# Performance work log

Hardware: AMD Instinct MI355X
Metric: run time of the kernel (lower is better)

Reference implementation:

```python
import jax, jax.numpy as jnp
import numpy as np

B, L, D = 16, 8192, 256

def setup_inputs() -> dict:
    key = jax.random.key(0)
    inputs = jax.random.normal(key, (B, L, D), dtype=jnp.float32)
    return {"inputs": inputs}

def reference(inputs) -> jnp.ndarray:
    # position weights: softmax over L of per-token L2 norms
    norms = jnp.linalg.norm(inputs, axis=2)            # [B, L]
    w = jax.nn.softmax(norms, axis=1)                  # [B, L]
    # weighted sum of outer products == X^T diag(w) X, fused as one einsum
    out = jnp.einsum('bl,bld,ble->bde', w, inputs, inputs)  # [B, D, D]
    return out
```

## Files before the change

kernel.cpp:

```cpp
#include <hip/hip_runtime.h>
#include <hip/hip_bf16.h>

#define NB 16
#define NL 8192
#define ND 256
#define KSPLIT 16
#define CHUNK (NL / KSPLIT)
#define BK 64

#define WS_G_OFF 256

typedef __bf16 bf16_t;
typedef __attribute__((ext_vector_type(8))) __bf16 bf16x8;
typedef __attribute__((ext_vector_type(4))) float floatx4;

__device__ __forceinline__ int fsw(int col) {
    return ((col >> 2) & 7) ^ ((col & 3) << 1);
}

__global__ __launch_bounds__(512, 2) void k_gemm(const float* __restrict__ x,
                                                 float* __restrict__ ws,
                                                 float* __restrict__ gram) {
    const int ks = blockIdx.x, b = blockIdx.y;
    const int t = threadIdx.x;
    const int lane = t & 63;
    const int w = __builtin_amdgcn_readfirstlane(t >> 6);
    const int quad = lane >> 4, m = lane & 15;

    __shared__ bf16_t lds[256 * 64];

    const float* xb = x + (size_t)b * NL * ND;
    const int l0 = ks * CHUNK;

    floatx4 accA[9], accB[8];
    #pragma unroll
    for (int j = 0; j < 9; ++j)
        #pragma unroll
        for (int r = 0; r < 4; ++r) accA[j][r] = 0.f;
    #pragma unroll
    for (int j = 0; j < 8; ++j)
        #pragma unroll
        for (int r = 0; r < 4; ++r) accB[j][r] = 0.f;

    float e_acc = 0.f;
    float4 xv[8];

    {
        const float* gp = xb + (size_t)(l0 + w * 8) * ND + lane * 4;
        #pragma unroll
        for (int j = 0; j < 8; ++j) xv[j] = *(const float4*)(gp + (size_t)j * ND);
    }

    for (int kk = 0; kk < CHUNK; kk += BK) {
        if (kk) __syncthreads();
        {
            float ss[8];
            #pragma unroll
            for (int j = 0; j < 8; ++j)
                ss[j] = xv[j].x * xv[j].x + xv[j].y * xv[j].y
                      + xv[j].z * xv[j].z + xv[j].w * xv[j].w;
            #pragma unroll
            for (int off = 32; off; off >>= 1) {
                #pragma unroll
                for (int j = 0; j < 8; ++j) ss[j] += __shfl_xor(ss[j], off, 64);
            }
            float s[8];
            #pragma unroll
            for (int j = 0; j < 8; ++j) {
                s[j] = __expf(0.5f * sqrtf(ss[j]));
                e_acc += s[j] * s[j];
            }
            bf16x8 p[4];
            #pragma unroll
            for (int j = 0; j < 8; ++j) {
                const float* vf = (const float*)&xv[j];
                #pragma unroll
                for (int c = 0; c < 4; ++c) p[c][j] = (bf16_t)(vf[c] * s[j]);
            }
            #pragma unroll
            for (int c = 0; c < 4; ++c) {
                const int col = 4 * lane + c;
                const int chunk = w ^ fsw(col);
                *(bf16x8*)(&lds[col * 64 + chunk * 8]) = p[c];
            }
        }
        __syncthreads();
        if (kk + BK < CHUNK) {
            const float* gp = xb + (size_t)(l0 + kk + BK + w * 8) * ND + lane * 4;
            #pragma unroll
            for (int j = 0; j < 8; ++j) xv[j] = *(const float4*)(gp + (size_t)j * ND);
        }
        #pragma unroll
        for (int k2 = 0; k2 < 2; ++k2) {
            const int kcq = k2 * 4 + quad;
            bf16x8 fB[16];
            #pragma unroll
            for (int j = 0; j < 16; ++j) {
                const int col = (((w + j) & 15) << 4) + m;
                fB[j] = *(const bf16x8*)(&lds[(col << 6) + ((kcq ^ fsw(col)) << 3)]);
            }
            #pragma unroll
            for (int j = 0; j < 9; ++j)
                accA[j] = __builtin_amdgcn_mfma_f32_16x16x32_bf16(fB[0], fB[j], accA[j], 0, 0, 0);
            #pragma unroll
            for (int j = 0; j < 8; ++j)
                accB[j] = __builtin_amdgcn_mfma_f32_16x16x32_bf16(fB[8], fB[8 + j], accB[j], 0, 0, 0);
        }
    }

    __shared__ float red[8];
    if (lane == 0) red[w] = e_acc;
    __syncthreads();
    if (t == 0) {
        float z = 0.f;
        #pragma unroll
        for (int i = 0; i < 8; ++i) z += red[i];
        atomicAdd(&ws[b * 16], z);
    }

    float* gb = gram + (size_t)(ks * NB + b) * 144 * 256;
    #pragma unroll
    for (int j = 0; j < 9; ++j) {
        float* tb = gb + (w * 9 + j) * 256 + quad * 64 + m;
        #pragma unroll
        for (int reg = 0; reg < 4; ++reg) tb[reg * 16] = accA[j][reg];
    }
    #pragma unroll
    for (int j = 0; j < 8; ++j) {
        float* tb = gb + ((w + 8) * 9 + j) * 256 + quad * 64 + m;
        #pragma unroll
        for (int reg = 0; reg < 4; ++reg) tb[reg * 16] = accB[j][reg];
    }
}

__global__ __launch_bounds__(256) void k_reduce(const float* __restrict__ gram,
                                                const float* __restrict__ ws,
                                                float* __restrict__ out) {
    const int gid = blockIdx.x * 256 + threadIdx.x;
    const int elem = gid & 255;
    const int rem  = gid >> 8;
    const int slot = rem % 144;
    const int b    = rem / 144;
    const int rt = slot / 9;
    const int j  = slot - rt * 9;
    if (rt >= 8 && j == 8) return;
    const int ct = (rt + j) & 15;
    float sum = 0.f;
    #pragma unroll
    for (int ks = 0; ks < KSPLIT; ++ks)
        sum += gram[((size_t)(ks * NB + b) * 144 + slot) * 256 + elem];
    sum *= 1.0f / ws[b * 16];
    const int er = elem >> 4, ec = elem & 15;
    const int d = rt * 16 + er, e = ct * 16 + ec;
    float* ob = out + (size_t)b * ND * ND;
    ob[(size_t)d * ND + e] = sum;
    if (j) ob[(size_t)e * ND + d] = sum;
}

extern "C" void kernel_launch(void* const* d_in, const int* in_sizes, int n_in,
                              void* d_out, int out_size, void* d_ws, size_t ws_size,
                              hipStream_t stream) {
    const float* x = (const float*)d_in[0];
    float* out = (float*)d_out;
    float* ws = (float*)d_ws;
    float* gram = ws + WS_G_OFF;

    hipMemsetAsync(d_ws, 0, 1024, stream);
    k_gemm<<<dim3(KSPLIT, NB), 512, 0, stream>>>(x, ws, gram);
    k_reduce<<<dim3(NB * 144 * 256 / 256), 256, 0, stream>>>(gram, ws, out);
}
```

Baseline: 207.7 us.

## Double block to 1024 threads with one row-tile per wave

The GEMM kernel now launches 1024 threads (16 waves) instead of 512. Each wave owns a single 16-row tile with 9 accumulators, where before it owned two tiles with 17. Each wave loads 4 rows instead of 8 and writes bf16x4 halves into the swizzled LDS tile, and B fragments are loaded and consumed one at a time instead of being held as 16 registers. The aim is lower register pressure and more waves to hide latency. In exchange, upper-half waves now compute a redundant ninth (diagonal-opposite) tile, and the reduce kernel is adjusted to write it without transposing.

```diff
diff --git a/kernel.cpp b/kernel.cpp
--- a/kernel.cpp
+++ b/kernel.cpp
@@ -11,6 +11,7 @@
 #define WS_G_OFF 256
 
 typedef __bf16 bf16_t;
+typedef __attribute__((ext_vector_type(4))) __bf16 bf16x4;
 typedef __attribute__((ext_vector_type(8))) __bf16 bf16x8;
 typedef __attribute__((ext_vector_type(4))) float floatx4;
 
@@ -18,61 +19,57 @@
     return ((col >> 2) & 7) ^ ((col & 3) << 1);
 }
 
-__global__ __launch_bounds__(512, 2) void k_gemm(const float* __restrict__ x,
-                                                 float* __restrict__ ws,
-                                                 float* __restrict__ gram) {
+__global__ __launch_bounds__(1024, 4) void k_gemm(const float* __restrict__ x,
+                                                  float* __restrict__ ws,
+                                                  float* __restrict__ gram) {
     const int ks = blockIdx.x, b = blockIdx.y;
     const int t = threadIdx.x;
     const int lane = t & 63;
     const int w = __builtin_amdgcn_readfirstlane(t >> 6);
     const int quad = lane >> 4, m = lane & 15;
+    const int g = w >> 1, h = w & 1;
 
     __shared__ bf16_t lds[256 * 64];
 
     const float* xb = x + (size_t)b * NL * ND;
     const int l0 = ks * CHUNK;
 
-    floatx4 accA[9], accB[8];
+    floatx4 acc[9];
     #pragma unroll
     for (int j = 0; j < 9; ++j)
         #pragma unroll
-        for (int r = 0; r < 4; ++r) accA[j][r] = 0.f;
-    #pragma unroll
-    for (int j = 0; j < 8; ++j)
-        #pragma unroll
-        for (int r = 0; r < 4; ++r) accB[j][r] = 0.f;
+        for (int r = 0; r < 4; ++r) acc[j][r] = 0.f;
 
     float e_acc = 0.f;
-    float4 xv[8];
-
+    float4 xv[4];
     {
-        const float* gp = xb + (size_t)(l0 + w * 8) * ND + lane * 4;
+        const float* gp = xb + (size_t)(l0 + w * 4) * ND + lane * 4;
         #pragma unroll
-        for (int j = 0; j < 8; ++j) xv[j] = *(const float4*)(gp + (size_t)j * ND);
+        for (int j = 0; j < 4; ++j) xv[j] = *(const float4*)(gp + (size_t)j * ND);
     }
 
     for (int kk = 0; kk < CHUNK; kk += BK) {
         if (kk) __syncthreads();
         {
-            float ss[8];
+            float ss[4];
             #pragma unroll
-            for (int j = 0; j < 8; ++j)
+            for (int j = 0; j < 4; ++j)
                 ss[j] = xv[j].x * xv[j].x + xv[j].y * xv[j].y
                       + xv[j].z * xv[j].z + xv[j].w * xv[j].w;
             #pragma unroll
             for (int off = 32; off; off >>= 1) {
                 #pragma unroll
-                for (int j = 0; j < 8; ++j) ss[j] += __shfl_xor(ss[j], off, 64);
+                for (int j = 0; j < 4; ++j) ss[j] += __shfl_xor(ss[j], off, 64);
             }
-            float s[8];
+            float s[4];
             #pragma unroll
-            for (int j = 0; j < 8; ++j) {
+            for (int j = 0; j < 4; ++j) {
                 s[j] = __expf(0.5f * sqrtf(ss[j]));
                 e_acc += s[j] * s[j];
             }
-            bf16x8 p[4];
+            bf16x4 p[4];
             #pragma unroll
-            for (int j = 0; j < 8; ++j) {
+            for (int j = 0; j < 4; ++j) {
                 const float* vf = (const float*)&xv[j];
                 #pragma unroll
                 for (int c = 0; c < 4; ++c) p[c][j] = (bf16_t)(vf[c] * s[j]);
@@ -80,41 +77,36 @@
             #pragma unroll
             for (int c = 0; c < 4; ++c) {
                 const int col = 4 * lane + c;
-                const int chunk = w ^ fsw(col);
-                *(bf16x8*)(&lds[col * 64 + chunk * 8]) = p[c];
+                *(bf16x4*)(&lds[col * 64 + ((g ^ fsw(col)) << 3) + (h << 2)]) = p[c];
             }
         }
         __syncthreads();
         if (kk + BK < CHUNK) {
-            const float* gp = xb + (size_t)(l0 + kk + BK + w * 8) * ND + lane * 4;
+            const float* gp = xb + (size_t)(l0 + kk + BK + w * 4) * ND + lane * 4;
             #pragma unroll
-            for (int j = 0; j < 8; ++j) xv[j] = *(const float4*)(gp + (size_t)j * ND);
+            for (int j = 0; j < 4; ++j) xv[j] = *(const float4*)(gp + (size_t)j * ND);
         }
         #pragma unroll
         for (int k2 = 0; k2 < 2; ++k2) {
             const int kcq = k2 * 4 + quad;
-            bf16x8 fB[16];
+            const int col0 = (w << 4) + m;
+            const bf16x8 f0 = *(const bf16x8*)(&lds[(col0 << 6) + ((kcq ^ fsw(col0)) << 3)]);
             #pragma unroll
-            for (int j = 0; j < 16; ++j) {
+            for (int j = 0; j < 9; ++j) {
                 const int col = (((w + j) & 15) << 4) + m;
-                fB[j] = *(const bf16x8*)(&lds[(col << 6) + ((kcq ^ fsw(col)) << 3)]);
+                const bf16x8 fj = *(const bf16x8*)(&lds[(col << 6) + ((kcq ^ fsw(col)) << 3)]);
+                acc[j] = __builtin_amdgcn_mfma_f32_16x16x32_bf16(f0, fj, acc[j], 0, 0, 0);
             }
-            #pragma unroll
-            for (int j = 0; j < 9; ++j)
-                accA[j] = __builtin_amdgcn_mfma_f32_16x16x32_bf16(fB[0], fB[j], accA[j], 0, 0, 0);
-            #pragma unroll
-            for (int j = 0; j < 8; ++j)
-                accB[j] = __builtin_amdgcn_mfma_f32_16x16x32_bf16(fB[8], fB[8 + j], accB[j], 0, 0, 0);
         }
     }
 
-    __shared__ float red[8];
+    __shared__ float red[16];
     if (lane == 0) red[w] = e_acc;
     __syncthreads();
     if (t == 0) {
         float z = 0.f;
         #pragma unroll
-        for (int i = 0; i < 8; ++i) z += red[i];
+        for (int i = 0; i < 16; ++i) z += red[i];
         atomicAdd(&ws[b * 16], z);
     }
 
@@ -123,13 +115,7 @@
     for (int j = 0; j < 9; ++j) {
         float* tb = gb + (w * 9 + j) * 256 + quad * 64 + m;
         #pragma unroll
-        for (int reg = 0; reg < 4; ++reg) tb[reg * 16] = accA[j][reg];
-    }
-    #pragma unroll
-    for (int j = 0; j < 8; ++j) {
-        float* tb = gb + ((w + 8) * 9 + j) * 256 + quad * 64 + m;
-        #pragma unroll
-        for (int reg = 0; reg < 4; ++reg) tb[reg * 16] = accB[j][reg];
+        for (int reg = 0; reg < 4; ++reg) tb[reg * 16] = acc[j][reg];
     }
 }
 
@@ -143,7 +129,6 @@
     const int b    = rem / 144;
     const int rt = slot / 9;
     const int j  = slot - rt * 9;
-    if (rt >= 8 && j == 8) return;
     const int ct = (rt + j) & 15;
     float sum = 0.f;
     #pragma unroll
@@ -154,7 +139,7 @@
     const int d = rt * 16 + er, e = ct * 16 + ec;
     float* ob = out + (size_t)b * ND * ND;
     ob[(size_t)d * ND + e] = sum;
-    if (j) ob[(size_t)e * ND + d] = sum;
+    if (j >= 1 && j <= 7) ob[(size_t)e * ND + d] = sum;
 }
 
 extern "C" void kernel_launch(void* const* d_in, const int* in_sizes, int n_in,
@@ -166,6 +151,6 @@
     float* gram = ws + WS_G_OFF;
 
     hipMemsetAsync(d_ws, 0, 1024, stream);
-    k_gemm<<<dim3(KSPLIT, NB), 512, 0, stream>>>(x, ws, gram);
+    k_gemm<<<dim3(KSPLIT, NB), 1024, 0, stream>>>(x, ws, gram);
     k_reduce<<<dim3(NB * 144 * 256 / 256), 256, 0, stream>>>(gram, ws, out);
 }
```

Result: no change. 207.2 us (-0.2%).
